# Kernel optimization log

Hardware: AMD Instinct MI355X
Metric: run time of the kernel (lower is better)

## Reference

```python
import jax, jax.numpy as jnp
import numpy as np

B, L, D, E, H, FFN_MULT = 16, 2048, 512, 8, 8, 4
HD = D // H
ALPHA, BETA, LN_EPS = 1.0, 0.5, 1e-5


def _ln(x, g, b):
    mu = x.mean(-1, keepdims=True)
    var = ((x - mu) ** 2).mean(-1, keepdims=True)
    return (x - mu) * jax.lax.rsqrt(var + LN_EPS) * g + b


def setup_inputs() -> dict:
    key = jax.random.key(0)
    ks = jax.random.split(key, 20)
    s = 0.02
    return {
        "query": jax.random.normal(ks[0], (B, D), jnp.float32),
        "retrieved": jax.random.normal(ks[1], (B, L, D), jnp.float32),
        "w_gate": jax.random.normal(ks[2], (D, E), jnp.float32) * s,
        "ln_q_g": jnp.ones((E, D), jnp.float32),
        "ln_q_b": jnp.zeros((E, D), jnp.float32),
        "Wq": jax.random.normal(ks[3], (E, D, D), jnp.float32) * s,
        "bq": jnp.zeros((E, D), jnp.float32),
        "Wk": jax.random.normal(ks[4], (E, D, D), jnp.float32) * s,
        "bk": jnp.zeros((E, D), jnp.float32),
        "Wv": jax.random.normal(ks[5], (E, D, D), jnp.float32) * s,
        "bv": jnp.zeros((E, D), jnp.float32),
        "Wo": jax.random.normal(ks[6], (E, D, D), jnp.float32) * s,
        "bo": jnp.zeros((E, D), jnp.float32),
        "ln_o_g": jnp.ones((E, D), jnp.float32),
        "ln_o_b": jnp.zeros((E, D), jnp.float32),
        "W1": jax.random.normal(ks[7], (E, D, FFN_MULT * D), jnp.float32) * s,
        "b1": jnp.zeros((E, FFN_MULT * D), jnp.float32),
        "W2": jax.random.normal(ks[8], (E, FFN_MULT * D, D), jnp.float32) * s,
        "b2": jnpp_zeros((E, D)) if False else jnp.zeros((E, D), jnp.float32),
    }


def reference(query, retrieved, w_gate, ln_q_g, ln_q_b, Wq, bq, Wk, bk, Wv, bv,
              Wo, bo, ln_o_g, ln_o_b, W1, b1, W2, b2):
    # Gating (eval mode: no noise, r=None) -> (B, E)
    gates = jax.nn.softmax(query @ w_gate, axis=-1)

    # Per-expert LayerNorm of the (shared) query: normalize once, affine per expert
    mu = query.mean(-1, keepdims=True)
    var = ((query - mu) ** 2).mean(-1, keepdims=True)
    xn = (query - mu) * jax.lax.rsqrt(var + LN_EPS)              # (B, D)
    qn = xn[:, None, :] * ln_q_g[None] + ln_q_b[None]            # (B, E, D)

    # Cross-attention, query length 1, per expert (MHA with in/out proj)
    qh = (jnp.einsum('bed,edk->bek', qn, Wq) + bq).reshape(B, E, H, HD)
    k = (jnp.einsum('bld,edk->belk', retrieved, Wk) + bk[:, None, :]).reshape(B, E, L, H, HD)
    v = (jnp.einsum('bld,edk->belk', retrieved, Wv) + bv[:, None, :]).reshape(B, E, L, H, HD)
    scores = jnp.einsum('behc,belhc->behl', qh, k) / jnp.sqrt(jnp.float32(HD))
    probs = jax.nn.softmax(scores, axis=-1)                      # (B, E, H, L)
    attn = jnp.einsum('behl,belhc->behc', probs, v).reshape(B, E, D)
    attn_out = jnp.einsum('bed,edk->bek', attn, Wo) + bo         # (B, E, D)
    avg_probs = probs.mean(axis=2)                               # (B, E, L) heads averaged

    # Residual + FFN (dropouts inactive at eval)
    x = query[:, None, :] + attn_out                             # (B, E, D)
    xo = _ln(x, ln_o_g[None], ln_o_b[None])
    h = jax.nn.gelu(jnp.einsum('bed,edf->bef', xo, W1) + b1, approximate=False)
    y = jnp.einsum('bef,efd->bed', h, W2) + b2 + x               # expert_outs (B, E, D)

    # Entropy-derived reliability
    p = jnp.clip(avg_probs, 1e-12, None)
    Hent = -(p * jnp.log(p)).sum(-1)                             # (B, E)
    s_all = jnp.exp(-BETA * Hent)

    gt = gates * s_all
    gt = gt / (gt.sum(-1, keepdims=True) + 1e-9)
    mixture = (gt[..., None] * y).sum(1)                         # (B, D)
    fused = ALPHA * mixture + (1.0 - ALPHA) * query
    return fused, y, gt
```

## Files before the change

### kernel.cpp

```cpp
#include <hip/hip_runtime.h>
#include <math.h>

#define CB 16
#define CL 2048
#define CD 512
#define CE 8
#define CH 8
#define CEH 64
#define CF 2048

typedef __bf16 bf16x8 __attribute__((ext_vector_type(8)));
typedef float f32x4 __attribute__((ext_vector_type(4)));

#define GLL16(srcp, dstp) __builtin_amdgcn_global_load_lds( \
    (const __attribute__((address_space(1))) unsigned int*)(srcp), \
    (__attribute__((address_space(3))) unsigned int*)(dstp), 16, 0, 0)

#define WS_GATES 0
#define WS_XN    (WS_GATES + CB*CE)
#define WS_QN    (WS_XN + CB*CD)
#define WS_QH    (WS_QN + CB*CE*CD)
#define WS_SBIAS (WS_QH + CB*CE*CD)
#define WS_WK    (WS_SBIAS + CB*CE*CH)
#define WS_SC    (WS_WK + CB*CEH*CD)
#define WS_PART  WS_SC
#define WS_RMAX  (WS_SC + CB*CL*CEH)
#define WS_RINV  (WS_RMAX + CB*CEH)
#define WS_ENT   (WS_RINV + CB*CEH)
#define WS_ATTN  (WS_ENT + CB*CE*8)
#define WS_X     (WS_ATTN + CB*CE*CD)
#define WS_XO    (WS_X + CB*CE*CD)
#define WS_HB    (WS_XO + CB*CE*CD)
#define WS_RP    (WS_HB + CB*CE*CF)
#define WS_PB16  (WS_RP + 8*CB*CEH*CD)

__global__ __launch_bounds__(256) void k1_gates_xn(
    const float* __restrict__ q, const float* __restrict__ wg,
    float* __restrict__ xn, float* __restrict__ gates) {
  int b = blockIdx.x, t = threadIdx.x;
  __shared__ float red[256];
  __shared__ float logits[CE];
  float v0 = q[b*CD + t], v1 = q[b*CD + 256 + t];
  red[t] = v0 + v1; __syncthreads();
  for (int s = 128; s > 0; s >>= 1) { if (t < s) red[t] += red[t+s]; __syncthreads(); }
  float mu = red[0] * (1.0f/CD); __syncthreads();
  float c0 = v0 - mu, c1 = v1 - mu;
  red[t] = c0*c0 + c1*c1; __syncthreads();
  for (int s = 128; s > 0; s >>= 1) { if (t < s) red[t] += red[t+s]; __syncthreads(); }
  float rstd = rsqrtf(red[0] * (1.0f/CD) + 1e-5f); __syncthreads();
  xn[b*CD + t] = c0 * rstd;
  xn[b*CD + 256 + t] = c1 * rstd;
  float ge[CE];
  #pragma unroll
  for (int e = 0; e < CE; e++) ge[e] = v0 * wg[t*CE + e] + v1 * wg[(256+t)*CE + e];
  for (int e = 0; e < CE; e++) {
    red[t] = ge[e]; __syncthreads();
    for (int s = 128; s > 0; s >>= 1) { if (t < s) red[t] += red[t+s]; __syncthreads(); }
    if (t == 0) logits[e] = red[0];
    __syncthreads();
  }
  if (t == 0) {
    float m = logits[0];
    for (int e = 1; e < CE; e++) m = fmaxf(m, logits[e]);
    float s = 0.f, ex[CE];
    for (int e = 0; e < CE; e++) { ex[e] = __expf(logits[e] - m); s += ex[e]; }
    for (int e = 0; e < CE; e++) gates[b*CE + e] = ex[e] / s;
  }
}

__global__ __launch_bounds__(256) void k1b_qn(
    const float* __restrict__ xn, const float* __restrict__ g,
    const float* __restrict__ bln, float* __restrict__ qn) {
  int i = blockIdx.x*256 + threadIdx.x;
  int b = i >> 12, e = (i >> 9) & 7, d = i & 511;
  qn[i] = xn[b*CD + d] * g[e*CD + d] + bln[e*CD + d];
}

template<int KC>
__global__ __launch_bounds__(256) void gstream(
    const float* __restrict__ X, int xb_, int xe_,
    const float* __restrict__ W, size_t we_, int ldw,
    float* __restrict__ P, int ntiles, size_t pc_, int pb_, int pe_) {
  int e = blockIdx.y;
  int nt = blockIdx.x % ntiles, kc = blockIdx.x / ntiles;
  int n0 = nt * 64, k0 = kc * KC;
  __shared__ float xs[KC][16];
  __shared__ float red[16][64];
  int t = threadIdx.x;
  for (int idx = t; idx < KC * 16; idx += 256) {
    int k = idx >> 4, b = idx & 15;
    xs[k][b] = X[(size_t)b * xb_ + (size_t)e * xe_ + k0 + k];
  }
  __syncthreads();
  int n = t & 63, kq = t >> 6;
  float acc[16] = {};
  const float* Wp = W + (size_t)e * we_ + (size_t)k0 * ldw + n0 + n;
  #pragma unroll 4
  for (int k = kq * (KC/4); k < (kq+1) * (KC/4); k++) {
    float w = Wp[(size_t)k * ldw];
    const float4* xp = reinterpret_cast<const float4*>(xs[k]);
    float4 x0 = xp[0], x1 = xp[1], x2 = xp[2], x3 = xp[3];
    acc[0]  += x0.x*w; acc[1]  += x0.y*w; acc[2]  += x0.z*w; acc[3]  += x0.w*w;
    acc[4]  += x1.x*w; acc[5]  += x1.y*w; acc[6]  += x1.z*w; acc[7]  += x1.w*w;
    acc[8]  += x2.x*w; acc[9]  += x2.y*w; acc[10] += x2.z*w; acc[11] += x2.w*w;
    acc[12] += x3.x*w; acc[13] += x3.y*w; acc[14] += x3.z*w; acc[15] += x3.w*w;
  }
  if (kq == 0) {
    #pragma unroll
    for (int b = 0; b < 16; b++) red[b][n] = acc[b];
  }
  __syncthreads();
  #pragma unroll
  for (int qq = 1; qq < 4; qq++) {
    if (kq == qq) {
      #pragma unroll
      for (int b = 0; b < 16; b++) red[b][n] += acc[b];
    }
    __syncthreads();
  }
  #pragma unroll
  for (int i = 0; i < 4; i++) {
    int b = kq*4 + i;
    P[(size_t)kc*pc_ + (size_t)b*pb_ + (size_t)e*pe_ + n0 + n] = red[b][n];
  }
}

__global__ __launch_bounds__(256) void gstream_v(
    const float* __restrict__ rp, const float* __restrict__ Wv,
    float* __restrict__ P) {
  int eh = blockIdx.y, kc = blockIdx.x;
  int e = eh >> 3, h = eh & 7;
  int k0 = kc * 64;
  __shared__ float xs[64][20];
  __shared__ float red[16][64];
  int t = threadIdx.x;
  for (int idx = t; idx < 64 * 16; idx += 256) {
    int k = idx & 63, b = idx >> 6;
    float s = 0.f;
    #pragma unroll
    for (int c = 0; c < 8; c++)
      s += rp[(size_t)c*(CB*CEH*CD) + ((size_t)(b*CEH + eh))*CD + k0 + k];
    xs[k][b] = s;
  }
  __syncthreads();
  int n = t & 63, kq = t >> 6;
  float acc[16] = {};
  const float* Wp = Wv + (size_t)e*CD*CD + (size_t)k0*CD + h*64 + n;
  #pragma unroll 4
  for (int k = kq*16; k < kq*16 + 16; k++) {
    float w = Wp[(size_t)k * CD];
    const float4* xp = reinterpret_cast<const float4*>(&xs[k][0]);
    float4 x0 = xp[0], x1 = xp[1], x2 = xp[2], x3 = xp[3];
    acc[0]  += x0.x*w; acc[1]  += x0.y*w; acc[2]  += x0.z*w; acc[3]  += x0.w*w;
    acc[4]  += x1.x*w; acc[5]  += x1.y*w; acc[6]  += x1.z*w; acc[7]  += x1.w*w;
    acc[8]  += x2.x*w; acc[9]  += x2.y*w; acc[10] += x2.z*w; acc[11] += x2.w*w;
    acc[12] += x3.x*w; acc[13] += x3.y*w; acc[14] += x3.z*w; acc[15] += x3.w*w;
  }
  if (kq == 0) { 
    #pragma unroll
    for (int b = 0; b < 16; b++) red[b][n] = acc[b]; }
  __syncthreads();
  #pragma unroll
  for (int qq = 1; qq < 4; qq++) {
    if (kq == qq) {
      #pragma unroll
      for (int b = 0; b < 16; b++) red[b][n] += acc[b];
    }
    __syncthreads();
  }
  #pragma unroll
  for (int i = 0; i < 4; i++) {
    int b = kq*4 + i;
    P[(size_t)kc*65536 + (size_t)b*4096 + (size_t)eh*64 + n] = red[b][n];
  }
}

__global__ __launch_bounds__(256) void comb8_bias(
    const float* __restrict__ P, const float* __restrict__ bias,
    float* __restrict__ out) {
  int i = blockIdx.x*256 + threadIdx.x;
  float s = bias[i & 4095];
  #pragma unroll
  for (int c = 0; c < 8; c++) s += P[(size_t)c*65536 + i];
  out[i] = s;
}

__global__ __launch_bounds__(256) void comb8_o(
    const float* __restrict__ P, const float* __restrict__ bias,
    const float* __restrict__ q, float* __restrict__ x) {
  int i = blockIdx.x*256 + threadIdx.x;
  float s = bias[i & 4095] + q[(i >> 12)*CD + (i & 511)];
  #pragma unroll
  for (int c = 0; c < 8; c++) s += P[(size_t)c*65536 + i];
  x[i] = s;
}

__global__ __launch_bounds__(256) void comb4_gelu(
    const float* __restrict__ P, const float* __restrict__ bias,
    float* __restrict__ out) {
  int i = blockIdx.x*256 + threadIdx.x;
  float s = bias[i & 16383];
  #pragma unroll
  for (int c = 0; c < 4; c++) s += P[(size_t)c*262144 + i];
  out[i] = 0.5f*s*(1.f + erff(s*0.70710678118f));
}

__global__ __launch_bounds__(256) void comb8_ffn2(
    const float* __restrict__ P, const float* __restrict__ bias,
    const float* __restrict__ x, float* __restrict__ yout) {
  int i = blockIdx.x*256 + threadIdx.x;
  float s = bias[i & 4095] + x[i];
  #pragma unroll
  for (int c = 0; c < 8; c++) s += P[(size_t)c*65536 + i];
  yout[i] = s;
}

__global__ __launch_bounds__(64) void k3_sbias(
    const float* __restrict__ qh, const float* __restrict__ bk,
    float* __restrict__ sbias) {
  int be = blockIdx.x, b = be >> 3, e = be & 7, t = threadIdx.x;
  for (int h = 0; h < CH; h++) {
    float v = qh[(b*CE + e)*CD + h*64 + t] * bk[e*CD + h*64 + t];
    for (int off = 32; off > 0; off >>= 1) v += __shfl_down(v, off);
    if (t == 0) sbias[(b*CE + e)*CH + h] = v;
  }
}

__global__ __launch_bounds__(256) void k4_wkeff(
    const float* __restrict__ Wk, const float* __restrict__ qh,
    __bf16* __restrict__ wkh) {
  int e = blockIdx.y;
  int h = blockIdx.x >> 3, dt = blockIdx.x & 7;
  int d0 = dt * 64;
  __shared__ float wks[64][65];
  __shared__ float qs[64][16];
  __shared__ float red[16][64];
  int t = threadIdx.x;
  for (int idx = t; idx < 64*64; idx += 256) {
    int c = idx & 63, d = idx >> 6;
    wks[c][d] = Wk[(size_t)e*CD*CD + (size_t)(d0+d)*CD + h*64 + c];
  }
  for (int idx = t; idx < 64*16; idx += 256) {
    int c = idx >> 4, b = idx & 15;
    qs[c][b] = qh[(b*CE + e)*CD + h*64 + c];
  }
  __syncthreads();
  int d = t & 63, cq = t >> 6;
  float acc[16] = {};
  #pragma unroll 4
  for (int c = cq*16; c < cq*16 + 16; c++) {
    float w = wks[c][d];
    const float4* xp = reinterpret_cast<const float4*>(qs[c]);
    float4 x0 = xp[0], x1 = xp[1], x2 = xp[2], x3 = xp[3];
    acc[0]  += x0.x*w; acc[1]  += x0.y*w; acc[2]  += x0.z*w; acc[3]  += x0.w*w;
    acc[4]  += x1.x*w; acc[5]  += x1.y*w; acc[6]  += x1.z*w; acc[7]  += x1.w*w;
    acc[8]  += x2.x*w; acc[9]  += x2.y*w; acc[10] += x2.z*w; acc[11] += x2.w*w;
    acc[12] += x3.x*w; acc[13] += x3.y*w; acc[14] += x3.z*w; acc[15] += x3.w*w;
  }
  if (cq == 0) { 
    #pragma unroll
    for (int b = 0; b < 16; b++) red[b][d] = acc[b]; }
  __syncthreads();
  #pragma unroll
  for (int qq = 1; qq < 4; qq++) {
    if (cq == qq) {
      #pragma unroll
      for (int b = 0; b < 16; b++) red[b][d] += acc[b];
    }
    __syncthreads();
  }
  int eh = e*8 + h;
  #pragma unroll
  for (int i = 0; i < 4; i++) {
    int b = cq*4 + i;
    wkh[((size_t)(b*CEH + eh))*CD + d0 + d] = (__bf16)red[b][d];
  }
}

__global__ __launch_bounds__(256) void k5_mfma(
    const float* __restrict__ ret, const __bf16* __restrict__ wkh,
    const float* __restrict__ sbias, float* __restrict__ sc,
    float* __restrict__ lmax, float* __restrict__ lsum) {
  int b = blockIdx.y, lt = blockIdx.x, t = threadIdx.x;
  int w = t >> 6, lane = t & 63;
  int lnlo = lane & 15, lnhi = lane >> 4;
  int lh = w & 1, ehh = w >> 1;
  int l0blk = lt*32;
  int ehbase = ehh*32;
  __shared__ __align__(16) char ldsbuf[32768];
  f32x4 acc[2];
  acc[0] = (f32x4){0.f,0.f,0.f,0.f};
  acc[1] = (f32x4){0.f,0.f,0.f,0.f};
  const float*  retb  = ret + (size_t)(b*CL + l0blk)*CD;
  const __bf16* wkhb  = wkh + (size_t)b*CEH*CD;

  int rs0 = t,        rl0 = rs0 >> 4, rg0 = ((rs0 & 15) ^ (rl0 & 15)) << 2;
  int rs1 = t + 256,  rl1 = rs1 >> 4, rg1 = ((rs1 & 15) ^ (rl1 & 15)) << 2;
  int ws0 = t,        we0 = ws0 >> 3, wg0 = ((ws0 & 7) ^ (we0 & 7)) << 3;
  int ws1 = t + 256,  we1 = ws1 >> 3, wg1 = ((ws1 & 7) ^ (we1 & 7)) << 3;

  #define K5_STAGE(bufi, kt) do {                                          \
    char* rB = ldsbuf + (bufi)*8192;                                       \
    char* wB = ldsbuf + 16384 + (bufi)*8192;                               \
    int dofs = (kt)*64;                                                    \
    GLL16(retb + (size_t)rl0*CD + dofs + rg0, rB + rs0*16);                \
    GLL16(retb + (size_t)rl1*CD + dofs + rg1, rB + rs1*16);                \
    GLL16(wkhb + (size_t)we0*CD + dofs + wg0, wB + ws0*16);                \
    GLL16(wkhb + (size_t)we1*CD + dofs + wg1, wB + ws1*16);                \
  } while (0)

  K5_STAGE(0, 0);
  __syncthreads();
  #pragma unroll
  for (int kt = 0; kt < 8; kt++) {
    int cur = kt & 1;
    if (kt < 7) K5_STAGE(cur ^ 1, kt + 1);
    const char* rB = ldsbuf + cur*8192;
    const char* wB = ldsbuf + 16384 + cur*8192;
    #pragma unroll
    for (int sub = 0; sub < 2; sub++) {
      int g0 = (sub*8 + lnhi*2 + 0) ^ lnlo;
      int g1 = (sub*8 + lnhi*2 + 1) ^ lnlo;
      float4 f0 = *reinterpret_cast<const float4*>(rB + (lh*16 + lnlo)*256 + g0*16);
      float4 f1 = *reinterpret_cast<const float4*>(rB + (lh*16 + lnlo)*256 + g1*16);
      bf16x8 bfrag;
      bfrag[0]=(__bf16)f0.x; bfrag[1]=(__bf16)f0.y; bfrag[2]=(__bf16)f0.z; bfrag[3]=(__bf16)f0.w;
      bfrag[4]=(__bf16)f1.x; bfrag[5]=(__bf16)f1.y; bfrag[6]=(__bf16)f1.z; bfrag[7]=(__bf16)f1.w;
      int ga = (sub*4 + lnhi) ^ (lnlo & 7);
      bf16x8 a0 = *reinterpret_cast<const bf16x8*>(wB + (ehbase + 0*16 + lnlo)*128 + ga*16);
      bf16x8 a1 = *reinterpret_cast<const bf16x8*>(wB + (ehbase + 1*16 + lnlo)*128 + ga*16);
      acc[0] = __builtin_amdgcn_mfma_f32_16x16x32_bf16(a0, bfrag, acc[0], 0, 0, 0);
      acc[1] = __builtin_amdgcn_mfma_f32_16x16x32_bf16(a1, bfrag, acc[1], 0, 0, 0);
    }
    __syncthreads();
  }
  #undef K5_STAGE

  int strip = lt*2 + lh;
  int l = l0blk + lh*16 + lnlo;
  #pragma unroll
  for (int et = 0; et < 2; et++) {
    #pragma unroll
    for (int i = 0; i < 4; i++) {
      int eh = ehbase + et*16 + lnhi*4 + i;
      float v = acc[et][i]*0.125f + sbias[b*CEH + eh]*0.125f;
      sc[((size_t)(b*CEH + eh))*CL + l] = v;
      float m = v;
      m = fmaxf(m, __shfl_xor(m, 1));
      m = fmaxf(m, __shfl_xor(m, 2));
      m = fmaxf(m, __shfl_xor(m, 4));
      m = fmaxf(m, __shfl_xor(m, 8));
      float s = __expf(v - m);
      s += __shfl_xor(s, 1);
      s += __shfl_xor(s, 2);
      s += __shfl_xor(s, 4);
      s += __shfl_xor(s, 8);
      if (lnlo == et*4 + i) {
        lmax[((size_t)(b*CEH + eh))*128 + strip] = m;
        lsum[((size_t)(b*CEH + eh))*128 + strip] = s;
      }
    }
  }
}

__global__ __launch_bounds__(256) void k5b2(
    const float* __restrict__ lmax, const float* __restrict__ lsum,
    float* __restrict__ rmax, float* __restrict__ rinv) {
  int b = blockIdx.x, t = threadIdx.x, eh = t & 63, q = t >> 6;
  const float* lm = lmax + ((size_t)(b*CEH + eh))*128 + q*32;
  const float* ls = lsum + ((size_t)(b*CEH + eh))*128 + q*32;
  float M = -1e30f, S = 0.f;
  for (int i = 0; i < 32; i++) {
    float m2 = lm[i], s2 = ls[i];
    float Mn = fmaxf(M, m2);
    S = S*__expf(M - Mn) + s2*__expf(m2 - Mn);
    M = Mn;
  }
  __shared__ float sm[4][64], ss[4][64];
  sm[q][eh] = M; ss[q][eh] = S;
  __syncthreads();
  if (q == 0) {
    #pragma unroll
    for (int i = 1; i < 4; i++) {
      float m2 = sm[i][eh], s2 = ss[i][eh];
      float Mn = fmaxf(M, m2);
      S = S*__expf(M - Mn) + s2*__expf(m2 - Mn);
      M = Mn;
    }
    rmax[b*CEH + eh] = M;
    rinv[b*CEH + eh] = 1.f / S;
  }
}

__global__ __launch_bounds__(256) void k5n(
    const float* __restrict__ sc, const float* __restrict__ rmax,
    const float* __restrict__ rinv, __bf16* __restrict__ pb,
    float* __restrict__ entp) {
  int e = blockIdx.x, b = blockIdx.y, lc = blockIdx.z, t = threadIdx.x;
  int l = lc*256 + t;
  float pbav = 0.f;
  #pragma unroll
  for (int h = 0; h < 8; h++) {
    size_t ix = ((size_t)(b*CEH + e*8 + h))*CL + l;
    float p = __expf(sc[ix] - rmax[b*CEH + e*8 + h]) * rinv[b*CEH + e*8 + h];
    pb[ix] = (__bf16)p;
    pbav += p;
  }
  pbav = fmaxf(pbav*0.125f, 1e-12f);
  float ent = -pbav * __logf(pbav);
  __shared__ float red[256];
  red[t] = ent; __syncthreads();
  for (int s = 128; s > 0; s >>= 1) { if (t < s) red[t] += red[t+s]; __syncthreads(); }
  if (t == 0) entp[(b*CE + e)*8 + lc] = red[0];
}

__global__ __launch_bounds__(256) void k6_mfma(
    const __bf16* __restrict__ pb, const float* __restrict__ ret,
    float* __restrict__ part) {
  int b = blockIdx.y;
  int dt = blockIdx.x & 7, lc = blockIdx.x >> 3;
  int d0 = dt*64, l0 = lc*256;
  int t = threadIdx.x, w = t >> 6, lane = t & 63;
  int lnlo = lane & 15, lnhi = lane >> 4;
  __shared__ __bf16 Bs[2][64][40];
  f32x4 acc[4];
  #pragma unroll
  for (int et = 0; et < 4; et++) acc[et] = (f32x4){0.f,0.f,0.f,0.f};
  const __bf16* pbb = pb + ((size_t)(b*CEH) + lnlo)*CL + l0 + lnhi*8;
  int srow = t & 31, scol = (t >> 5)*8;
  const float* retb = ret + ((size_t)(b*CL) + l0 + srow)*CD + d0 + scol;
  float4 v0 = *reinterpret_cast<const float4*>(retb);
  float4 v1 = *reinterpret_cast<const float4*>(retb + 4);
  bf16x8 ap0 = *reinterpret_cast<const bf16x8*>(pbb);
  bf16x8 ap1 = *reinterpret_cast<const bf16x8*>(pbb + (size_t)16*CL);
  bf16x8 ap2 = *reinterpret_cast<const bf16x8*>(pbb + (size_t)32*CL);
  bf16x8 ap3 = *reinterpret_cast<const bf16x8*>(pbb + (size_t)48*CL);
  #pragma unroll
  for (int kt = 0; kt < 8; kt++) {
    int cur = kt & 1;
    Bs[cur][scol+0][srow] = (__bf16)v0.x; Bs[cur][scol+1][srow] = (__bf16)v0.y;
    Bs[cur][scol+2][srow] = (__bf16)v0.z; Bs[cur][scol+3][srow] = (__bf16)v0.w;
    Bs[cur][scol+4][srow] = (__bf16)v1.x; Bs[cur][scol+5][srow] = (__bf16)v1.y;
    Bs[cur][scol+6][srow] = (__bf16)v1.z; Bs[cur][scol+7][srow] = (__bf16)v1.w;
    bf16x8 an0, an1, an2, an3;
    if (kt < 7) {
      v0 = *reinterpret_cast<const float4*>(retb + (size_t)(kt+1)*32*CD);
      v1 = *reinterpret_cast<const float4*>(retb + (size_t)(kt+1)*32*CD + 4);
      an0 = *reinterpret_cast<const bf16x8*>(pbb + (kt+1)*32);
      an1 = *reinterpret_cast<const bf16x8*>(pbb + (size_t)16*CL + (kt+1)*32);
      an2 = *reinterpret_cast<const bf16x8*>(pbb + (size_t)32*CL + (kt+1)*32);
      an3 = *reinterpret_cast<const bf16x8*>(pbb + (size_t)48*CL + (kt+1)*32);
    }
    __syncthreads();
    bf16x8 bfrag = *reinterpret_cast<const bf16x8*>(&Bs[cur][w*16 + lnlo][lnhi*8]);
    acc[0] = __builtin_amdgcn_mfma_f32_16x16x32_bf16(ap0, bfrag, acc[0], 0, 0, 0);
    acc[1] = __builtin_amdgcn_mfma_f32_16x16x32_bf16(ap1, bfrag, acc[1], 0, 0, 0);
    acc[2] = __builtin_amdgcn_mfma_f32_16x16x32_bf16(ap2, bfrag, acc[2], 0, 0, 0);
    acc[3] = __builtin_amdgcn_mfma_f32_16x16x32_bf16(ap3, bfrag, acc[3], 0, 0, 0);
    if (kt < 7) { ap0 = an0; ap1 = an1; ap2 = an2; ap3 = an3; }
  }
  float* dst = part + (size_t)lc*(CB*CEH*CD);
  int d = d0 + w*16 + lnlo;
  #pragma unroll
  for (int et = 0; et < 4; et++) {
    #pragma unroll
    for (int i = 0; i < 4; i++) {
      int eh = et*16 + lnhi*4 + i;
      dst[((size_t)(b*CEH + eh))*CD + d] = acc[et][i];
    }
  }
}

__global__ __launch_bounds__(256) void k7_lno(
    const float* __restrict__ x, const float* __restrict__ g,
    const float* __restrict__ bb, float* __restrict__ xo) {
  int be = blockIdx.x, e = be & 7, t = threadIdx.x;
  __shared__ float red[256];
  const float* xr = x + (size_t)be*CD;
  float v0 = xr[t], v1 = xr[256 + t];
  red[t] = v0 + v1; __syncthreads();
  for (int s = 128; s > 0; s >>= 1) { if (t < s) red[t] += red[t+s]; __syncthreads(); }
  float mu = red[0] * (1.0f/CD); __syncthreads();
  float c0 = v0 - mu, c1 = v1 - mu;
  red[t] = c0*c0 + c1*c1; __syncthreads();
  for (int s = 128; s > 0; s >>= 1) { if (t < s) red[t] += red[t+s]; __syncthreads(); }
  float rstd = rsqrtf(red[0] * (1.0f/CD) + 1e-5f);
  xo[be*CD + t]       = c0*rstd*g[e*CD + t]       + bb[e*CD + t];
  xo[be*CD + 256 + t] = c1*rstd*g[e*CD + 256 + t] + bb[e*CD + 256 + t];
}

__global__ __launch_bounds__(512) void k10_final(
    const float* __restrict__ gates, const float* __restrict__ entp,
    const float* __restrict__ yout, float* __restrict__ fused,
    float* __restrict__ gtout) {
  int b = blockIdx.x, t = threadIdx.x;
  __shared__ float gt_s[CE];
  if (t < CE) {
    float Hs = 0.f;
    #pragma unroll
    for (int c = 0; c < 8; c++) Hs += entp[(b*CE + t)*8 + c];
    gt_s[t] = gates[b*CE + t] * __expf(-0.5f * Hs);
  }
  __syncthreads();
  if (t == 0) {
    float s = 0.f;
    for (int e = 0; e < CE; e++) s += gt_s[e];
    s += 1e-9f;
    for (int e = 0; e < CE; e++) { gt_s[e] /= s; gtout[b*CE + e] = gt_s[e]; }
  }
  __syncthreads();
  float acc = 0.f;
  #pragma unroll
  for (int e = 0; e < CE; e++) acc += gt_s[e] * yout[(b*CE + e)*CD + t];
  fused[b*CD + t] = acc;
}

extern "C" void kernel_launch(void* const* d_in, const int* in_sizes, int n_in,
                              void* d_out, int out_size, void* d_ws, size_t ws_size,
                              hipStream_t stream) {
  const float* q    = (const float*)d_in[0];
  const float* ret  = (const float*)d_in[1];
  const float* wg   = (const float*)d_in[2];
  const float* lnqg = (const float*)d_in[3];
  const float* lnqb = (const float*)d_in[4];
  const float* Wq   = (const float*)d_in[5];
  const float* bq   = (const float*)d_in[6];
  const float* Wk   = (const float*)d_in[7];
  const float* bk   = (const float*)d_in[8];
  const float* Wv   = (const float*)d_in[9];
  const float* bv   = (const float*)d_in[10];
  const float* Wo   = (const float*)d_in[11];
  const float* bo   = (const float*)d_in[12];
  const float* lnog = (const float*)d_in[13];
  const float* lnob = (const float*)d_in[14];
  const float* W1   = (const float*)d_in[15];
  const float* b1   = (const float*)d_in[16];
  const float* W2   = (const float*)d_in[17];
  const float* b2   = (const float*)d_in[18];

  float* ws = (float*)d_ws;
  float* fused = (float*)d_out;
  float* yout  = fused + CB*CD;
  float* gtout = yout + CB*CE*CD;

  float* gates = ws + WS_GATES;
  float* xn    = ws + WS_XN;
  float* qn    = ws + WS_QN;
  float* qh    = ws + WS_QH;
  float* sbias = ws + WS_SBIAS;
  __bf16* wkh  = (__bf16*)(ws + WS_WK);
  float* sc    = ws + WS_SC;
  float* part  = ws + WS_PART;
  float* rmax  = ws + WS_RMAX;
  float* rinv  = ws + WS_RINV;
  float* entp  = ws + WS_ENT;
  float* attn  = ws + WS_ATTN;
  float* xb    = ws + WS_X;
  float* xo    = ws + WS_XO;
  float* hbuf  = ws + WS_HB;
  float* rpart = ws + WS_RP;
  __bf16* pb16 = (__bf16*)(ws + WS_PB16);
  float* lmax  = rpart;
  float* lsum  = rpart + CB*CEH*128;

  k1_gates_xn<<<CB, 256, 0, stream>>>(q, wg, xn, gates);
  k1b_qn<<<256, 256, 0, stream>>>(xn, lnqg, lnqb, qn);
  gstream<64><<<dim3(64, CE), 256, 0, stream>>>(qn, CE*CD, CD, Wq, (size_t)CD*CD, CD,
                                                part, 8, 65536, CE*CD, CD);
  comb8_bias<<<256, 256, 0, stream>>>(part, bq, qh);
  k3_sbias<<<CB*CE, 64, 0, stream>>>(qh, bk, sbias);
  k4_wkeff<<<dim3(64, CE), 256, 0, stream>>>(Wk, qh, wkh);
  k5_mfma<<<dim3(64, CB), 256, 0, stream>>>(ret, wkh, sbias, sc, lmax, lsum);
  k5b2<<<CB, 256, 0, stream>>>(lmax, lsum, rmax, rinv);
  k5n<<<dim3(CE, CB, 8), 256, 0, stream>>>(sc, rmax, rinv, pb16, entp);
  k6_mfma<<<dim3(64, CB), 256, 0, stream>>>(pb16, ret, rpart);
  gstream_v<<<dim3(8, CEH), 256, 0, stream>>>(rpart, Wv, part);
  comb8_bias<<<256, 256, 0, stream>>>(part, bv, attn);
  gstream<64><<<dim3(64, CE), 256, 0, stream>>>(attn, CE*CD, CD, Wo, (size_t)CD*CD, CD,
                                                part, 8, 65536, CE*CD, CD);
  comb8_o<<<256, 256, 0, stream>>>(part, bo, q, xb);
  k7_lno<<<CB*CE, 256, 0, stream>>>(xb, lnog, lnob, xo);
  gstream<128><<<dim3(128, CE), 256, 0, stream>>>(xo, CE*CD, CD, W1, (size_t)CD*CF, CF,
                                                  part, 32, 262144, CE*CF, CF);
  comb4_gelu<<<1024, 256, 0, stream>>>(part, b1, hbuf);
  gstream<256><<<dim3(64, CE), 256, 0, stream>>>(hbuf, CE*CF, CF, W2, (size_t)CF*CD, CD,
                                                 part, 8, 65536, CE*CD, CD);
  comb8_ffn2<<<256, 256, 0, stream>>>(part, b2, xb, yout);
  k10_final<<<CB, 512, 0, stream>>>(gates, entp, yout, fused, gtout);
}
```

Baseline: 137.9 us.

## Fuse split-K combine epilogues into neighbouring kernels to cut launches

```diff
diff --git a/kernel.cpp b/kernel.cpp
--- a/kernel.cpp
+++ b/kernel.cpp
@@ -24,6 +24,7 @@
 #define WS_WK    (WS_SBIAS + CB*CE*CH)
 #define WS_SC    (WS_WK + CB*CEH*CD)
 #define WS_PART  WS_SC
+#define WS_PART1 (WS_PART + 524288)
 #define WS_RMAX  (WS_SC + CB*CL*CEH)
 #define WS_RINV  (WS_RMAX + CB*CEH)
 #define WS_ENT   (WS_RINV + CB*CEH)
@@ -34,9 +35,10 @@
 #define WS_RP    (WS_HB + CB*CE*CF)
 #define WS_PB16  (WS_RP + 8*CB*CEH*CD)
 
-__global__ __launch_bounds__(256) void k1_gates_xn(
+__global__ __launch_bounds__(256) void k1_gates_qn(
     const float* __restrict__ q, const float* __restrict__ wg,
-    float* __restrict__ xn, float* __restrict__ gates) {
+    const float* __restrict__ g, const float* __restrict__ bln,
+    float* __restrict__ qn, float* __restrict__ gates) {
   int b = blockIdx.x, t = threadIdx.x;
   __shared__ float red[256];
   __shared__ float logits[CE];
@@ -48,8 +50,12 @@
   red[t] = c0*c0 + c1*c1; __syncthreads();
   for (int s = 128; s > 0; s >>= 1) { if (t < s) red[t] += red[t+s]; __syncthreads(); }
   float rstd = rsqrtf(red[0] * (1.0f/CD) + 1e-5f); __syncthreads();
-  xn[b*CD + t] = c0 * rstd;
-  xn[b*CD + 256 + t] = c1 * rstd;
+  float xn0 = c0 * rstd, xn1 = c1 * rstd;
+  #pragma unroll
+  for (int e = 0; e < CE; e++) {
+    qn[(b*CE + e)*CD + t]       = xn0 * g[e*CD + t]       + bln[e*CD + t];
+    qn[(b*CE + e)*CD + 256 + t] = xn1 * g[e*CD + 256 + t] + bln[e*CD + 256 + t];
+  }
   float ge[CE];
   #pragma unroll
   for (int e = 0; e < CE; e++) ge[e] = v0 * wg[t*CE + e] + v1 * wg[(256+t)*CE + e];
@@ -66,14 +72,6 @@
     for (int e = 0; e < CE; e++) { ex[e] = __expf(logits[e] - m); s += ex[e]; }
     for (int e = 0; e < CE; e++) gates[b*CE + e] = ex[e] / s;
   }
-}
-
-__global__ __launch_bounds__(256) void k1b_qn(
-    const float* __restrict__ xn, const float* __restrict__ g,
-    const float* __restrict__ bln, float* __restrict__ qn) {
-  int i = blockIdx.x*256 + threadIdx.x;
-  int b = i >> 12, e = (i >> 9) & 7, d = i & 511;
-  qn[i] = xn[b*CD + d] * g[e*CD + d] + bln[e*CD + d];
 }
 
 template<int KC>
@@ -175,24 +173,92 @@
   }
 }
 
-__global__ __launch_bounds__(256) void comb8_bias(
-    const float* __restrict__ P, const float* __restrict__ bias,
-    float* __restrict__ out) {
-  int i = blockIdx.x*256 + threadIdx.x;
-  float s = bias[i & 4095];
-  #pragma unroll
-  for (int c = 0; c < 8; c++) s += P[(size_t)c*65536 + i];
-  out[i] = s;
-}
-
-__global__ __launch_bounds__(256) void comb8_o(
-    const float* __restrict__ P, const float* __restrict__ bias,
-    const float* __restrict__ q, float* __restrict__ x) {
-  int i = blockIdx.x*256 + threadIdx.x;
-  float s = bias[i & 4095] + q[(i >> 12)*CD + (i & 511)];
-  #pragma unroll
-  for (int c = 0; c < 8; c++) s += P[(size_t)c*65536 + i];
-  x[i] = s;
+__global__ __launch_bounds__(256) void gstream_wo(
+    const float* __restrict__ Pv, const float* __restrict__ bv,
+    const float* __restrict__ Wo, float* __restrict__ P) {
+  int e = blockIdx.y;
+  int nt = blockIdx.x % 8, kc = blockIdx.x / 8;
+  int n0 = nt * 64, k0 = kc * 64;
+  __shared__ float xs[64][20];
+  __shared__ float red[16][64];
+  int t = threadIdx.x;
+  for (int idx = t; idx < 64 * 16; idx += 256) {
+    int k = idx & 63, b = idx >> 6;
+    float s = bv[e*CD + k0 + k];
+    #pragma unroll
+    for (int c = 0; c < 8; c++)
+      s += Pv[(size_t)c*65536 + (size_t)b*4096 + e*512 + k0 + k];
+    xs[k][b] = s;
+  }
+  __syncthreads();
+  int n = t & 63, kq = t >> 6;
+  float acc[16] = {};
+  const float* Wp = Wo + (size_t)e*CD*CD + (size_t)k0*CD + n0 + n;
+  #pragma unroll 4
+  for (int k = kq*16; k < kq*16 + 16; k++) {
+    float w = Wp[(size_t)k * CD];
+    const float4* xp = reinterpret_cast<const float4*>(&xs[k][0]);
+    float4 x0 = xp[0], x1 = xp[1], x2 = xp[2], x3 = xp[3];
+    acc[0]  += x0.x*w; acc[1]  += x0.y*w; acc[2]  += x0.z*w; acc[3]  += x0.w*w;
+    acc[4]  += x1.x*w; acc[5]  += x1.y*w; acc[6]  += x1.z*w; acc[7]  += x1.w*w;
+    acc[8]  += x2.x*w; acc[9]  += x2.y*w; acc[10] += x2.z*w; acc[11] += x2.w*w;
+    acc[12] += x3.x*w; acc[13] += x3.y*w; acc[14] += x3.z*w; acc[15] += x3.w*w;
+  }
+  if (kq == 0) {
+    #pragma unroll
+    for (int b = 0; b < 16; b++) red[b][n] = acc[b]; }
+  __syncthreads();
+  #pragma unroll
+  for (int qq = 1; qq < 4; qq++) {
+    if (kq == qq) {
+      #pragma unroll
+      for (int b = 0; b < 16; b++) red[b][n] += acc[b];
+    }
+    __syncthreads();
+  }
+  #pragma unroll
+  for (int i = 0; i < 4; i++) {
+    int b = kq*4 + i;
+    P[(size_t)kc*65536 + (size_t)b*4096 + (size_t)e*512 + n0 + n] = red[b][n];
+  }
+}
+
+__global__ __launch_bounds__(512) void comb_qh_sbias(
+    const float* __restrict__ P, const float* __restrict__ bq,
+    const float* __restrict__ bk, float* __restrict__ qh,
+    float* __restrict__ sbias) {
+  int be = blockIdx.x, b = be >> 3, e = be & 7, t = threadIdx.x;
+  float s = bq[e*CD + t];
+  #pragma unroll
+  for (int c = 0; c < 8; c++)
+    s += P[(size_t)c*65536 + (size_t)b*4096 + e*512 + t];
+  qh[be*CD + t] = s;
+  float w = s * bk[e*CD + t];
+  #pragma unroll
+  for (int off = 32; off > 0; off >>= 1) w += __shfl_down(w, off);
+  if ((t & 63) == 0) sbias[be*CH + (t >> 6)] = w;
+}
+
+__global__ __launch_bounds__(512) void comb_o_lno(
+    const float* __restrict__ P, const float* __restrict__ bo,
+    const float* __restrict__ q, const float* __restrict__ g,
+    const float* __restrict__ bb, float* __restrict__ xb,
+    float* __restrict__ xo) {
+  int be = blockIdx.x, b = be >> 3, e = be & 7, t = threadIdx.x;
+  float v = q[b*CD + t] + bo[e*CD + t];
+  #pragma unroll
+  for (int c = 0; c < 8; c++)
+    v += P[(size_t)c*65536 + (size_t)b*4096 + e*512 + t];
+  xb[be*CD + t] = v;
+  __shared__ float red[512];
+  red[t] = v; __syncthreads();
+  for (int s = 256; s > 0; s >>= 1) { if (t < s) red[t] += red[t+s]; __syncthreads(); }
+  float mu = red[0] * (1.0f/CD); __syncthreads();
+  float c0 = v - mu;
+  red[t] = c0*c0; __syncthreads();
+  for (int s = 256; s > 0; s >>= 1) { if (t < s) red[t] += red[t+s]; __syncthreads(); }
+  float rstd = rsqrtf(red[0] * (1.0f/CD) + 1e-5f);
+  xo[be*CD + t] = c0*rstd*g[e*CD + t] + bb[e*CD + t];
 }
 
 __global__ __launch_bounds__(256) void comb4_gelu(
@@ -205,25 +271,39 @@
   out[i] = 0.5f*s*(1.f + erff(s*0.70710678118f));
 }
 
-__global__ __launch_bounds__(256) void comb8_ffn2(
-    const float* __restrict__ P, const float* __restrict__ bias,
-    const float* __restrict__ x, float* __restrict__ yout) {
-  int i = blockIdx.x*256 + threadIdx.x;
-  float s = bias[i & 4095] + x[i];
-  #pragma unroll
-  for (int c = 0; c < 8; c++) s += P[(size_t)c*65536 + i];
-  yout[i] = s;
-}
-
-__global__ __launch_bounds__(64) void k3_sbias(
-    const float* __restrict__ qh, const float* __restrict__ bk,
-    float* __restrict__ sbias) {
-  int be = blockIdx.x, b = be >> 3, e = be & 7, t = threadIdx.x;
-  for (int h = 0; h < CH; h++) {
-    float v = qh[(b*CE + e)*CD + h*64 + t] * bk[e*CD + h*64 + t];
-    for (int off = 32; off > 0; off >>= 1) v += __shfl_down(v, off);
-    if (t == 0) sbias[(b*CE + e)*CH + h] = v;
-  }
+__global__ __launch_bounds__(512) void comb_ffn2_final(
+    const float* __restrict__ P, const float* __restrict__ b2,
+    const float* __restrict__ xb, const float* __restrict__ gates,
+    const float* __restrict__ entp, float* __restrict__ yout,
+    float* __restrict__ fused, float* __restrict__ gtout) {
+  int b = blockIdx.x, t = threadIdx.x;
+  __shared__ float gt_s[CE];
+  if (t < CE) {
+    float Hs = 0.f;
+    #pragma unroll
+    for (int c = 0; c < 8; c++) Hs += entp[(b*CE + t)*8 + c];
+    gt_s[t] = gates[b*CE + t] * __expf(-0.5f * Hs);
+  }
+  __syncthreads();
+  if (t == 0) {
+    float s = 0.f;
+    for (int e = 0; e < CE; e++) s += gt_s[e];
+    s += 1e-9f;
+    for (int e = 0; e < CE; e++) gt_s[e] /= s;
+  }
+  __syncthreads();
+  float acc = 0.f;
+  #pragma unroll
+  for (int e = 0; e < CE; e++) {
+    float y = b2[e*CD + t] + xb[(b*CE + e)*CD + t];
+    #pragma unroll
+    for (int c = 0; c < 8; c++)
+      y += P[(size_t)c*65536 + (size_t)b*4096 + e*512 + t];
+    yout[(b*CE + e)*CD + t] = y;
+    acc += gt_s[e] * y;
+  }
+  fused[b*CD + t] = acc;
+  if (t < CE) gtout[b*CE + t] = gt_s[t];
 }
 
 __global__ __launch_bounds__(256) void k4_wkeff(
@@ -469,50 +549,6 @@
       dst[((size_t)(b*CEH + eh))*CD + d] = acc[et][i];
     }
   }
-}
-
-__global__ __launch_bounds__(256) void k7_lno(
-    const float* __restrict__ x, const float* __restrict__ g,
-    const float* __restrict__ bb, float* __restrict__ xo) {
-  int be = blockIdx.x, e = be & 7, t = threadIdx.x;
-  __shared__ float red[256];
-  const float* xr = x + (size_t)be*CD;
-  float v0 = xr[t], v1 = xr[256 + t];
-  red[t] = v0 + v1; __syncthreads();
-  for (int s = 128; s > 0; s >>= 1) { if (t < s) red[t] += red[t+s]; __syncthreads(); }
-  float mu = red[0] * (1.0f/CD); __syncthreads();
-  float c0 = v0 - mu, c1 = v1 - mu;
-  red[t] = c0*c0 + c1*c1; __syncthreads();
-  for (int s = 128; s > 0; s >>= 1) { if (t < s) red[t] += red[t+s]; __syncthreads(); }
-  float rstd = rsqrtf(red[0] * (1.0f/CD) + 1e-5f);
-  xo[be*CD + t]       = c0*rstd*g[e*CD + t]       + bb[e*CD + t];
-  xo[be*CD + 256 + t] = c1*rstd*g[e*CD + 256 + t] + bb[e*CD + 256 + t];
-}
-
-__global__ __launch_bounds__(512) void k10_final(
-    const float* __restrict__ gates, const float* __restrict__ entp,
-    const float* __restrict__ yout, float* __restrict__ fused,
-    float* __restrict__ gtout) {
-  int b = blockIdx.x, t = threadIdx.x;
-  __shared__ float gt_s[CE];
-  if (t < CE) {
-    float Hs = 0.f;
-    #pragma unroll
-    for (int c = 0; c < 8; c++) Hs += entp[(b*CE + t)*8 + c];
-    gt_s[t] = gates[b*CE + t] * __expf(-0.5f * Hs);
-  }
-  __syncthreads();
-  if (t == 0) {
-    float s = 0.f;
-    for (int e = 0; e < CE; e++) s += gt_s[e];
-    s += 1e-9f;
-    for (int e = 0; e < CE; e++) { gt_s[e] /= s; gtout[b*CE + e] = gt_s[e]; }
-  }
-  __syncthreads();
-  float acc = 0.f;
-  #pragma unroll
-  for (int e = 0; e < CE; e++) acc += gt_s[e] * yout[(b*CE + e)*CD + t];
-  fused[b*CD + t] = acc;
 }
 
 extern "C" void kernel_launch(void* const* d_in, const int* in_sizes, int n_in,
@@ -544,17 +580,16 @@
   float* gtout = yout + CB*CE*CD;
 
   float* gates = ws + WS_GATES;
-  float* xn    = ws + WS_XN;
   float* qn    = ws + WS_QN;
   float* qh    = ws + WS_QH;
   float* sbias = ws + WS_SBIAS;
   __bf16* wkh  = (__bf16*)(ws + WS_WK);
   float* sc    = ws + WS_SC;
-  float* part  = ws + WS_PART;
+  float* part0 = ws + WS_PART;
+  float* part1 = ws + WS_PART1;
   float* rmax  = ws + WS_RMAX;
   float* rinv  = ws + WS_RINV;
   float* entp  = ws + WS_ENT;
-  float* attn  = ws + WS_ATTN;
   float* xb    = ws + WS_X;
   float* xo    = ws + WS_XO;
   float* hbuf  = ws + WS_HB;
@@ -563,28 +598,22 @@
   float* lmax  = rpart;
   float* lsum  = rpart + CB*CEH*128;
 
-  k1_gates_xn<<<CB, 256, 0, stream>>>(q, wg, xn, gates);
-  k1b_qn<<<256, 256, 0, stream>>>(xn, lnqg, lnqb, qn);
+  k1_gates_qn<<<CB, 256, 0, stream>>>(q, wg, lnqg, lnqb, qn, gates);
   gstream<64><<<dim3(64, CE), 256, 0, stream>>>(qn, CE*CD, CD, Wq, (size_t)CD*CD, CD,
-                                                part, 8, 65536, CE*CD, CD);
-  comb8_bias<<<256, 256, 0, stream>>>(part, bq, qh);
-  k3_sbias<<<CB*CE, 64, 0, stream>>>(qh, bk, sbias);
+                                                part0, 8, 65536, CE*CD, CD);
+  comb_qh_sbias<<<CB*CE, 512, 0, stream>>>(part0, bq, bk, qh, sbias);
   k4_wkeff<<<dim3(64, CE), 256, 0, stream>>>(Wk, qh, wkh);
   k5_mfma<<<dim3(64, CB), 256, 0, stream>>>(ret, wkh, sbias, sc, lmax, lsum);
   k5b2<<<CB, 256, 0, stream>>>(lmax, lsum, rmax, rinv);
   k5n<<<dim3(CE, CB, 8), 256, 0, stream>>>(sc, rmax, rinv, pb16, entp);
   k6_mfma<<<dim3(64, CB), 256, 0, stream>>>(pb16, ret, rpart);
-  gstream_v<<<dim3(8, CEH), 256, 0, stream>>>(rpart, Wv, part);
-  comb8_bias<<<256, 256, 0, stream>>>(part, bv, attn);
-  gstream<64><<<dim3(64, CE), 256, 0, stream>>>(attn, CE*CD, CD, Wo, (size_t)CD*CD, CD,
-                                                part, 8, 65536, CE*CD, CD);
-  comb8_o<<<256, 256, 0, stream>>>(part, bo, q, xb);
-  k7_lno<<<CB*CE, 256, 0, stream>>>(xb, lnog, lnob, xo);
+  gstream_v<<<dim3(8, CEH), 256, 0, stream>>>(rpart, Wv, part1);
+  gstream_wo<<<dim3(64, CE), 256, 0, stream>>>(part1, bv, Wo, part0);
+  comb_o_lno<<<CB*CE, 512, 0, stream>>>(part0, bo, q, lnog, lnob, xb, xo);
   gstream<128><<<dim3(128, CE), 256, 0, stream>>>(xo, CE*CD, CD, W1, (size_t)CD*CF, CF,
-                                                  part, 32, 262144, CE*CF, CF);
-  comb4_gelu<<<1024, 256, 0, stream>>>(part, b1, hbuf);
+                                                  part0, 32, 262144, CE*CF, CF);
+  comb4_gelu<<<1024, 256, 0, stream>>>(part0, b1, hbuf);
   gstream<256><<<dim3(64, CE), 256, 0, stream>>>(hbuf, CE*CF, CF, W2, (size_t)CF*CD, CD,
-                                                 part, 8, 65536, CE*CD, CD);
-  comb8_ffn2<<<256, 256, 0, stream>>>(part, b2, xb, yout);
-  k10_final<<<CB, 512, 0, stream>>>(gates, entp, yout, fused, gtout);
-}
+                                                 part0, 8, 65536, CE*CD, CD);
+  comb_ffn2_final<<<CB, 512, 0, stream>>>(part0, b2, xb, gates, entp, yout, fused, gtout);
+}
```

Measured after the change: 129.0 us. -6.4%, faster.
